# Kernel optimization log

Hardware: AMD Instinct MI355X
Metric: run time of the kernel (lower is better)

The kernel has to match this reference:

```python
import jax, jax.numpy as jnp
import numpy as np

H, DK = 16, 64
F = H * DK  # n_feat = 1024
B, T = 2, 2048


def setup_inputs() -> dict:
    key = jax.random.key(0)
    ks = jax.random.split(key, 11)
    mk = lambda k, sh: jax.random.normal(k, sh, dtype=jnp.float32)
    inp = {
        "query": mk(ks[0], (B, T, F)),
        "key": mk(ks[1], (B, T, F)),
        "value": mk(ks[2], (B, T, F)),
    }
    # Standard RoPE frequency table, shaped [T,1,1,DK] to broadcast over [t,b,h,d].
    pos = jnp.arange(T, dtype=jnp.float32)[:, None]
    inv_freq = 1.0 / (10000.0 ** (jnp.arange(0, DK, 2, dtype=jnp.float32) / DK))
    ang = pos * inv_freq                       # [T, DK/2]
    emb = jnp.concatenate([ang, ang], axis=-1)  # [T, DK]
    inp["cos"] = jnp.cos(emb)[:, None, None, :]
    inp["sin"] = jnp.sin(emb)[:, None, None, :]
    scale = 1.0 / np.sqrt(F).astype(np.float32)
    for i, n in enumerate(["wq", "wk", "wv", "wo"]):
        inp[n] = mk(ks[3 + i], (F, F)) * scale  # torch Linear weight layout [out,in]
    for i, n in enumerate(["bq", "bk", "bv", "bo"]):
        inp[n] = mk(ks[7 + i], (F,)) * 0.01
    return inp


def _rtt_half(x):
    d = x.shape[-1]
    return jnp.concatenate([-x[..., d // 2:], x[..., :d // 2]], axis=-1)


def reference(query, key, value, cos, sin, wq, bq, wk, bk, wv, bv, wo, bo):
    b, t, f = query.shape
    h, d = H, DK
    # [b,t,f] -> [t,b,h,d] as in the torch code (RoPE applied pre-projection)
    to_tbhd = lambda x: jnp.swapaxes(x, 0, 1).reshape(t, b, h, d)
    q = to_tbhd(query)
    k = to_tbhd(key)
    c, s = cos[:t], sin[:t]
    q = q * c + _rtt_half(q) * s
    k = k * c + _rtt_half(k) * s
    back = lambda x: jnp.swapaxes(x.reshape(t, b, f), 0, 1)  # -> [b,t,f]
    q, k = back(q), back(k)
    lin = lambda x, w, bias: x @ w.T + bias
    Q = lin(q, wq, bq).reshape(b, t, h, d)
    K = lin(k, wk, bk).reshape(b, t, h, d)
    V = lin(value, wv, bv).reshape(b, t, h, d)
    scores = jnp.einsum('bqhd,bkhd->bhqk', Q, K) / jnp.sqrt(jnp.float32(d))
    attn = jax.nn.softmax(scores, axis=-1)
    o = jnp.einsum('bhqk,bkhd->bqhd', attn, V).reshape(b, t, f)
    return o @ wo.T + bo
```

## Files before the change

### kernel.cpp

```cpp
#include <hip/hip_runtime.h>
#include <hip/hip_bf16.h>

#define DEVI __device__ __forceinline__

typedef unsigned short u16;
typedef unsigned int u32;
typedef __attribute__((ext_vector_type(8))) short bf16x8;
typedef __attribute__((ext_vector_type(4))) short bf16x4;
typedef __attribute__((ext_vector_type(4))) float f32x4;

#define Bn 2
#define Tn 2048
#define Hn 16
#define Dn 64
#define Fn 1024

DEVI u16 tobf(float f) {
    __hip_bfloat16 h = __float2bfloat16(f);
    return __builtin_bit_cast(u16, h);
}
DEVI float frombf(u16 u) {
    return __builtin_bit_cast(float, ((u32)u) << 16);
}

DEVI f32x4 mfma16(bf16x8 a, bf16x8 b, f32x4 c) {
    return __builtin_amdgcn_mfma_f32_16x16x32_bf16(a, b, c, 0, 0, 0);
}

DEVI void gload_lds16(const u16* g, u16* l) {
    __builtin_amdgcn_global_load_lds(
        (const __attribute__((address_space(1))) void*)g,
        (__attribute__((address_space(3))) void*)l, 16, 0, 0);
}

__global__ __launch_bounds__(256) void k_prep(const float* __restrict__ q,
                                              const float* __restrict__ k,
                                              const float* __restrict__ v,
                                              const float* __restrict__ cosb,
                                              const float* __restrict__ sinb,
                                              const float* __restrict__ wq,
                                              const float* __restrict__ wk,
                                              const float* __restrict__ wv,
                                              const float* __restrict__ wo,
                                              u16* __restrict__ Aq,
                                              u16* __restrict__ Ak,
                                              u16* __restrict__ Av) {
    if (blockIdx.x < 4096) {
        unsigned idx = blockIdx.x * 256 + threadIdx.x;
        unsigned which = idx >> 19;
        unsigned r = idx & 0x7FFFFu;
        unsigned d0 = (r & 7u) << 2;
        unsigned h = (r >> 3) & 15u;
        unsigned t = (r >> 7) & 2047u;
        unsigned b = (r >> 18) & 1u;
        const float* src = which ? k : q;
        u16* dst = which ? Ak : Aq;
        size_t base = ((size_t)(b * Tn + t)) * Fn + h * Dn;
        float4 lo = *(const float4*)(src + base + d0);
        float4 hi = *(const float4*)(src + base + d0 + 32);
        float4 cl = *(const float4*)(cosb + (size_t)t * Dn + d0);
        float4 ch = *(const float4*)(cosb + (size_t)t * Dn + d0 + 32);
        float4 sl = *(const float4*)(sinb + (size_t)t * Dn + d0);
        float4 sh = *(const float4*)(sinb + (size_t)t * Dn + d0 + 32);
        bf16x4 olo, ohi;
        olo[0] = (short)tobf(lo.x * cl.x - hi.x * sl.x);
        olo[1] = (short)tobf(lo.y * cl.y - hi.y * sl.y);
        olo[2] = (short)tobf(lo.z * cl.z - hi.z * sl.z);
        olo[3] = (short)tobf(lo.w * cl.w - hi.w * sl.w);
        ohi[0] = (short)tobf(hi.x * ch.x + lo.x * sh.x);
        ohi[1] = (short)tobf(hi.y * ch.y + lo.y * sh.y);
        ohi[2] = (short)tobf(hi.z * ch.z + lo.z * sh.z);
        ohi[3] = (short)tobf(hi.w * ch.w + lo.w * sh.w);
        *(bf16x4*)(dst + base + d0) = olo;
        *(bf16x4*)(dst + base + d0 + 32) = ohi;
    } else {
        size_t i8 = (((size_t)blockIdx.x - 4096) * 256 + threadIdx.x) * 8;
        const size_t M4 = (size_t)4 << 20, M1 = (size_t)1 << 20;
        const float* src;
        size_t off;
        if (i8 < M4)              { src = v;  off = i8; }
        else if (i8 < M4 + M1)    { src = wq; off = i8 - M4; }
        else if (i8 < M4 + 2*M1)  { src = wk; off = i8 - M4 - M1; }
        else if (i8 < M4 + 3*M1)  { src = wv; off = i8 - M4 - 2*M1; }
        else                      { src = wo; off = i8 - M4 - 3*M1; }
        float4 a = *(const float4*)(src + off);
        float4 c = *(const float4*)(src + off + 4);
        bf16x8 vv;
        vv[0] = (short)tobf(a.x); vv[1] = (short)tobf(a.y);
        vv[2] = (short)tobf(a.z); vv[3] = (short)tobf(a.w);
        vv[4] = (short)tobf(c.x); vv[5] = (short)tobf(c.y);
        vv[6] = (short)tobf(c.z); vv[7] = (short)tobf(c.w);
        *(bf16x8*)(Av + i8) = vv;
    }
}

DEVI void store_out(u16* p, float v) { *p = tobf(v); }
DEVI void store_out(float* p, float v) { *p = v; }

template <typename OUT>
DEVI void gemm_body(const u16* __restrict__ A, const u16* __restrict__ W,
                    const float* __restrict__ bias, OUT* __restrict__ C,
                    float scale, u16* As, u16* Bs, int mode) {
    const int tid = threadIdx.x;
    const int lane = tid & 63;
    const int wave = tid >> 6;
    const int l15 = lane & 15, l4 = lane >> 4;
    const int bm = blockIdx.y << 7, bn = blockIdx.x << 7;
    const int wr = (wave >> 1) << 6, wc = (wave & 1) << 6;

    const int c0 = tid, c1 = tid + 256;
    const u16* A0p = A + (size_t)(bm + (c0 >> 2)) * 1024 + ((c0 & 3) << 3);
    const u16* A1p = A + (size_t)(bm + (c1 >> 2)) * 1024 + ((c1 & 3) << 3);
    const u16* B0p = W + (size_t)(bn + (c0 >> 2)) * 1024 + ((c0 & 3) << 3);
    const u16* B1p = W + (size_t)(bn + (c1 >> 2)) * 1024 + ((c1 & 3) << 3);
    u16* Ad0 = As + (c0 << 3);
    u16* Ad1 = As + (c1 << 3);
    u16* Bd0 = Bs + (c0 << 3);
    u16* Bd1 = Bs + (c1 << 3);

    f32x4 acc[4][4] = {};

    for (int k0 = 0; k0 < 1024; k0 += 32) {
        gload_lds16(A0p + k0, Ad0);
        gload_lds16(A1p + k0, Ad1);
        gload_lds16(B0p + k0, Bd0);
        gload_lds16(B1p + k0, Bd1);
        __syncthreads();
        bf16x8 af[4], bfr[4];
        #pragma unroll
        for (int m = 0; m < 4; m++)
            af[m] = *(const bf16x8*)(As + (wr + m * 16 + l15) * 32 + (l4 << 3));
        #pragma unroll
        for (int n = 0; n < 4; n++)
            bfr[n] = *(const bf16x8*)(Bs + (wc + n * 16 + l15) * 32 + (l4 << 3));
        #pragma unroll
        for (int m = 0; m < 4; m++)
            #pragma unroll
            for (int n = 0; n < 4; n++)
                acc[m][n] = mfma16(af[m], bfr[n], acc[m][n]);
        __syncthreads();
    }

    #pragma unroll
    for (int m = 0; m < 4; m++)
        #pragma unroll
        for (int n = 0; n < 4; n++) {
            const int gcol = bn + wc + n * 16 + l15;
            const float bb = bias[gcol];
            #pragma unroll
            for (int j = 0; j < 4; j++) {
                const int grow = bm + wr + m * 16 + (l4 << 2) + j;
                const float val = (acc[m][n][j] + bb) * scale;
                if (mode == 0) {
                    store_out(C + (size_t)grow * 1024 + gcol, val);
                } else {
                    const int b = grow >> 11, t = grow & 2047;
                    const int h = gcol >> 6, d = gcol & 63;
                    const int bh = b * 16 + h, tt2 = t >> 6, r = t & 63;
                    const size_t tbase = ((size_t)(bh * 32 + tt2)) << 12;
                    size_t off;
                    if (mode == 1) {
                        const int nn = ((r >> 5) << 1) | ((r >> 2) & 1);
                        const int kk = d >> 5, ll4 = (d >> 3) & 3, e = d & 7;
                        const int ll15 = (((r >> 3) & 3) << 2) | (r & 3);
                        off = tbase + ((size_t)(nn * 2 + kk) << 9) +
                              ((ll4 * 16 + ll15) << 3) + e;
                    } else {
                        const int kk = r >> 5, ll4 = (r >> 3) & 3, e = r & 7;
                        const int nd = d >> 4, ll15 = d & 15;
                        off = tbase + ((size_t)(kk * 4 + nd) << 9) +
                              ((ll4 * 16 + ll15) << 3) + e;
                    }
                    ((u16*)C)[off] = tobf(val);
                }
            }
        }
}

__global__ __launch_bounds__(256) void k_gemm_qkv(
    const u16* A0, const u16* W0, const float* b0, u16* C0,
    const u16* A1, const u16* W1, const float* b1, u16* C1,
    const u16* A2, const u16* W2, const float* b2, u16* C2) {
    __shared__ __align__(16) u16 As[128 * 32];
    __shared__ __align__(16) u16 Bs[128 * 32];
    const int z = blockIdx.z;
    const u16* A = z == 0 ? A0 : (z == 1 ? A1 : A2);
    const u16* W = z == 0 ? W0 : (z == 1 ? W1 : W2);
    const float* bias = z == 0 ? b0 : (z == 1 ? b1 : b2);
    u16* C = z == 0 ? C0 : (z == 1 ? C1 : C2);
    const float scale = z == 0 ? 0.125f * 1.4426950408889634f : 1.0f;
    gemm_body<u16>(A, W, bias, C, scale, As, Bs, z);
}

__global__ __launch_bounds__(256) void k_gemm_f32(const u16* __restrict__ A,
                                                  const u16* __restrict__ W,
                                                  const float* __restrict__ bias,
                                                  float* __restrict__ C) {
    __shared__ __align__(16) u16 As[128 * 32];
    __shared__ __align__(16) u16 Bs[128 * 32];
    gemm_body<float>(A, W, bias, C, 1.0f, As, Bs, 0);
}

__global__ __launch_bounds__(256) void k_attn(const u16* __restrict__ Qp,
                                              const u16* __restrict__ Kr,
                                              const u16* __restrict__ Vr,
                                              u16* __restrict__ Op0,
                                              u16* __restrict__ Op1,
                                              float* __restrict__ Ls) {
    const int tid = threadIdx.x, wave = tid >> 6, lane = tid & 63;
    const int l15 = lane & 15, l4 = lane >> 4;
    const int bh = blockIdx.x, b = bh >> 4, h = bh & 15;
    const int sp = blockIdx.z;
    const int q0 = blockIdx.y * 128 + wave * 32;
    const int tbase = sp << 4;

    bf16x8 aq[2][2];
    #pragma unroll
    for (int mq = 0; mq < 2; mq++)
        #pragma unroll
        for (int kk = 0; kk < 2; kk++)
            aq[mq][kk] = *(const bf16x8*)(Qp +
                ((size_t)(b * Tn + q0 + mq * 16 + l15)) * Fn + h * Dn + kk * 32 + (l4 << 3));

    f32x4 o[2][4] = {};
    float lrun[2] = {0.f, 0.f};

    bf16x8 ones;
    #pragma unroll
    for (int j = 0; j < 8; j++) ones[j] = (short)0x3F80;

    const u16* Kbr = Kr + ((size_t)bh << 17);
    const u16* Vbr = Vr + ((size_t)bh << 17);
    const int lo8 = lane * 8;

    bf16x8 ka[4][2];
    #pragma unroll
    for (int n = 0; n < 4; n++)
        #pragma unroll
        for (int kk = 0; kk < 2; kk++)
            ka[n][kk] = *(const bf16x8*)(Kbr + ((tbase * 8 + n * 2 + kk) << 9) + lo8);

    #pragma unroll 1
    for (int tt = 0; tt < 16; tt++) {
        const int tg = tbase + tt;
        bf16x8 va[2][4];
        #pragma unroll
        for (int kk = 0; kk < 2; kk++)
            #pragma unroll
            for (int nd = 0; nd < 4; nd++)
                va[kk][nd] = *(const bf16x8*)(Vbr + ((tg * 8 + kk * 4 + nd) << 9) + lo8);
        const int tn = (tt < 15) ? tg + 1 : tbase;
        bf16x8 kn[4][2];
        #pragma unroll
        for (int n = 0; n < 4; n++)
            #pragma unroll
            for (int kk = 0; kk < 2; kk++)
                kn[n][kk] = *(const bf16x8*)(Kbr + ((tn * 8 + n * 2 + kk) << 9) + lo8);

        f32x4 s[2][4] = {};
        __builtin_amdgcn_s_setprio(1);
        #pragma unroll
        for (int n = 0; n < 4; n++)
            #pragma unroll
            for (int kk = 0; kk < 2; kk++) {
                s[0][n] = mfma16(ka[n][kk], aq[0][kk], s[0][n]);
                s[1][n] = mfma16(ka[n][kk], aq[1][kk], s[1][n]);
            }
        __builtin_amdgcn_s_setprio(0);

        bf16x8 pb[2][2];
        #pragma unroll
        for (int mq = 0; mq < 2; mq++)
            #pragma unroll
            for (int kk = 0; kk < 2; kk++) {
                float p0 = __builtin_amdgcn_exp2f(s[mq][2 * kk][0]);
                float p1 = __builtin_amdgcn_exp2f(s[mq][2 * kk][1]);
                float p2 = __builtin_amdgcn_exp2f(s[mq][2 * kk][2]);
                float p3 = __builtin_amdgcn_exp2f(s[mq][2 * kk][3]);
                float p4 = __builtin_amdgcn_exp2f(s[mq][2 * kk + 1][0]);
                float p5 = __builtin_amdgcn_exp2f(s[mq][2 * kk + 1][1]);
                float p6 = __builtin_amdgcn_exp2f(s[mq][2 * kk + 1][2]);
                float p7 = __builtin_amdgcn_exp2f(s[mq][2 * kk + 1][3]);
                bf16x8 pv;
                pv[0] = (short)tobf(p0); pv[1] = (short)tobf(p1);
                pv[2] = (short)tobf(p2); pv[3] = (short)tobf(p3);
                pv[4] = (short)tobf(p4); pv[5] = (short)tobf(p5);
                pv[6] = (short)tobf(p6); pv[7] = (short)tobf(p7);
                pb[mq][kk] = pv;
            }

        f32x4 osum0 = {}, osum1 = {};
        __builtin_amdgcn_s_setprio(1);
        #pragma unroll
        for (int kk = 0; kk < 2; kk++) {
            #pragma unroll
            for (int nd = 0; nd < 4; nd++) {
                o[0][nd] = mfma16(va[kk][nd], pb[0][kk], o[0][nd]);
                o[1][nd] = mfma16(va[kk][nd], pb[1][kk], o[1][nd]);
            }
            osum0 = mfma16(ones, pb[0][kk], osum0);
            osum1 = mfma16(ones, pb[1][kk], osum1);
        }
        __builtin_amdgcn_s_setprio(0);
        lrun[0] += osum0[0];
        lrun[1] += osum1[0];

        #pragma unroll
        for (int n = 0; n < 4; n++) {
            ka[n][0] = kn[n][0];
            ka[n][1] = kn[n][1];
        }
    }

    u16* OpS = sp ? Op1 : Op0;
    #pragma unroll
    for (int mq = 0; mq < 2; mq++) {
        const int q = q0 + mq * 16 + l15;
        float inv = 1.f / lrun[mq];
        #pragma unroll
        for (int nd = 0; nd < 4; nd++) {
            bf16x4 ov;
            ov[0] = (short)tobf(o[mq][nd][0] * inv);
            ov[1] = (short)tobf(o[mq][nd][1] * inv);
            ov[2] = (short)tobf(o[mq][nd][2] * inv);
            ov[3] = (short)tobf(o[mq][nd][3] * inv);
            *(bf16x4*)(OpS + ((size_t)(b * Tn + q)) * Fn +
                       h * Dn + nd * 16 + (l4 << 2)) = ov;
        }
        if (l4 == 0)
            Ls[(((size_t)(sp * 2 + b)) * Tn + q) * Hn + h] = lrun[mq];
    }
}

__global__ __launch_bounds__(256) void k_combine(const u16* __restrict__ Op0,
                                                 const u16* __restrict__ Op1,
                                                 const float* __restrict__ Ls,
                                                 u16* __restrict__ Oa) {
    size_t e0 = ((size_t)blockIdx.x * 256 + threadIdx.x) * 8;
    int row = (int)(e0 >> 10);
    int b = row >> 11, q = row & 2047;
    int h = (int)(e0 >> 6) & 15;
    float l0 = Ls[(((size_t)(0 + b)) * Tn + q) * Hn + h];
    float l1 = Ls[(((size_t)(2 + b)) * Tn + q) * Hn + h];
    float inv = 1.f / (l0 + l1);
    float w0 = l0 * inv, w1 = l1 * inv;
    bf16x8 x0 = *(const bf16x8*)(Op0 + e0);
    bf16x8 x1 = *(const bf16x8*)(Op1 + e0);
    bf16x8 out;
    #pragma unroll
    for (int j = 0; j < 8; j++)
        out[j] = (short)tobf(frombf((u16)x0[j]) * w0 + frombf((u16)x1[j]) * w1);
    *(bf16x8*)(Oa + e0) = out;
}

extern "C" void kernel_launch(void* const* d_in, const int* in_sizes, int n_in,
                              void* d_out, int out_size, void* d_ws, size_t ws_size,
                              hipStream_t stream) {
    const float* q    = (const float*)d_in[0];
    const float* k    = (const float*)d_in[1];
    const float* v    = (const float*)d_in[2];
    const float* cosb = (const float*)d_in[3];
    const float* sinb = (const float*)d_in[4];
    const float* wq   = (const float*)d_in[5];
    const float* wk   = (const float*)d_in[6];
    const float* wv   = (const float*)d_in[7];
    const float* wo   = (const float*)d_in[8];
    const float* bq   = (const float*)d_in[9];
    const float* bk   = (const float*)d_in[10];
    const float* bv   = (const float*)d_in[11];
    const float* bo   = (const float*)d_in[12];

    char* ws = (char*)d_ws;
    const size_t MB = (size_t)1 << 20;
    u16* Aq  = (u16*)(ws);
    u16* Ak  = (u16*)(ws + 8 * MB);
    u16* Av  = (u16*)(ws + 16 * MB);
    u16* Wq  = (u16*)(ws + 24 * MB);
    u16* Wk  = (u16*)(ws + 26 * MB);
    u16* Wv  = (u16*)(ws + 28 * MB);
    u16* Wo  = (u16*)(ws + 30 * MB);
    u16* Qp  = (u16*)(ws + 32 * MB);
    u16* Kr  = (u16*)(ws + 40 * MB);
    u16* Vr  = (u16*)(ws + 48 * MB);
    float* Ls = (float*)Wq;
    u16* Op0 = Ak;
    u16* Op1 = Av;
    u16* Oa  = Aq;

    k_prep<<<8192, 256, 0, stream>>>(q, k, v, cosb, sinb, wq, wk, wv, wo,
                                     Aq, Ak, Av);
    k_gemm_qkv<<<dim3(8, 32, 3), 256, 0, stream>>>(Aq, Wq, bq, Qp,
                                                   Ak, Wk, bk, Kr,
                                                   Av, Wv, bv, Vr);
    k_attn<<<dim3(32, 16, 2), 256, 0, stream>>>(Qp, Kr, Vr, Op0, Op1, Ls);
    k_combine<<<2048, 256, 0, stream>>>(Op0, Op1, Ls, Oa);
    k_gemm_f32<<<dim3(8, 32), 256, 0, stream>>>(Oa, Wo, bo, (float*)d_out);
}
```

Measured before the change: 142.1 us.

## Split attention key range four ways and prefetch K directly into registers

The attention kernel now splits the key sequence into four chunks instead of two, doubling the grid and halving each block's loop length. The combine kernel merges four partial outputs weighted by their row sums. Partial buffers are relocated into the output buffer and freed workspace. The next K tile is loaded straight into the operand registers after the QK MFMAs, which removes the separate prefetch copy. The trade-off is more occupancy and parallelism against more partial-output traffic and a heavier combine pass.

```diff
diff --git a/kernel.cpp b/kernel.cpp
--- a/kernel.cpp
+++ b/kernel.cpp
@@ -206,13 +206,15 @@
                                               const u16* __restrict__ Vr,
                                               u16* __restrict__ Op0,
                                               u16* __restrict__ Op1,
+                                              u16* __restrict__ Op2,
+                                              u16* __restrict__ Op3,
                                               float* __restrict__ Ls) {
     const int tid = threadIdx.x, wave = tid >> 6, lane = tid & 63;
     const int l15 = lane & 15, l4 = lane >> 4;
     const int bh = blockIdx.x, b = bh >> 4, h = bh & 15;
     const int sp = blockIdx.z;
     const int q0 = blockIdx.y * 128 + wave * 32;
-    const int tbase = sp << 4;
+    const int tbase = sp << 3;
 
     bf16x8 aq[2][2];
     #pragma unroll
@@ -224,6 +226,7 @@
 
     f32x4 o[2][4] = {};
     float lrun[2] = {0.f, 0.f};
+    const f32x4 zero4 = {0.f, 0.f, 0.f, 0.f};
 
     bf16x8 ones;
     #pragma unroll
@@ -241,32 +244,32 @@
             ka[n][kk] = *(const bf16x8*)(Kbr + ((tbase * 8 + n * 2 + kk) << 9) + lo8);
 
     #pragma unroll 1
-    for (int tt = 0; tt < 16; tt++) {
+    for (int tt = 0; tt < 8; tt++) {
         const int tg = tbase + tt;
+        const int tn = (tt < 7) ? tg + 1 : tbase;
         bf16x8 va[2][4];
         #pragma unroll
         for (int kk = 0; kk < 2; kk++)
             #pragma unroll
             for (int nd = 0; nd < 4; nd++)
                 va[kk][nd] = *(const bf16x8*)(Vbr + ((tg * 8 + kk * 4 + nd) << 9) + lo8);
-        const int tn = (tt < 15) ? tg + 1 : tbase;
-        bf16x8 kn[4][2];
+
+        f32x4 s[2][4];
+        __builtin_amdgcn_s_setprio(1);
+        #pragma unroll
+        for (int n = 0; n < 4; n++) {
+            s[0][n] = mfma16(ka[n][0], aq[0][0], zero4);
+            s[1][n] = mfma16(ka[n][0], aq[1][0], zero4);
+            s[0][n] = mfma16(ka[n][1], aq[0][1], s[0][n]);
+            s[1][n] = mfma16(ka[n][1], aq[1][1], s[1][n]);
+        }
+        __builtin_amdgcn_s_setprio(0);
+
         #pragma unroll
         for (int n = 0; n < 4; n++)
             #pragma unroll
             for (int kk = 0; kk < 2; kk++)
-                kn[n][kk] = *(const bf16x8*)(Kbr + ((tn * 8 + n * 2 + kk) << 9) + lo8);
-
-        f32x4 s[2][4] = {};
-        __builtin_amdgcn_s_setprio(1);
-        #pragma unroll
-        for (int n = 0; n < 4; n++)
-            #pragma unroll
-            for (int kk = 0; kk < 2; kk++) {
-                s[0][n] = mfma16(ka[n][kk], aq[0][kk], s[0][n]);
-                s[1][n] = mfma16(ka[n][kk], aq[1][kk], s[1][n]);
-            }
-        __builtin_amdgcn_s_setprio(0);
+                ka[n][kk] = *(const bf16x8*)(Kbr + ((tn * 8 + n * 2 + kk) << 9) + lo8);
 
         bf16x8 pb[2][2];
         #pragma unroll
@@ -289,30 +292,24 @@
                 pb[mq][kk] = pv;
             }
 
-        f32x4 osum0 = {}, osum1 = {};
         __builtin_amdgcn_s_setprio(1);
-        #pragma unroll
-        for (int kk = 0; kk < 2; kk++) {
+        f32x4 osum0 = mfma16(ones, pb[0][0], zero4);
+        f32x4 osum1 = mfma16(ones, pb[1][0], zero4);
+        osum0 = mfma16(ones, pb[0][1], osum0);
+        osum1 = mfma16(ones, pb[1][1], osum1);
+        #pragma unroll
+        for (int kk = 0; kk < 2; kk++)
             #pragma unroll
             for (int nd = 0; nd < 4; nd++) {
                 o[0][nd] = mfma16(va[kk][nd], pb[0][kk], o[0][nd]);
                 o[1][nd] = mfma16(va[kk][nd], pb[1][kk], o[1][nd]);
             }
-            osum0 = mfma16(ones, pb[0][kk], osum0);
-            osum1 = mfma16(ones, pb[1][kk], osum1);
-        }
         __builtin_amdgcn_s_setprio(0);
         lrun[0] += osum0[0];
         lrun[1] += osum1[0];
-
-        #pragma unroll
-        for (int n = 0; n < 4; n++) {
-            ka[n][0] = kn[n][0];
-            ka[n][1] = kn[n][1];
-        }
     }
 
-    u16* OpS = sp ? Op1 : Op0;
+    u16* OpS = sp == 0 ? Op0 : (sp == 1 ? Op1 : (sp == 2 ? Op2 : Op3));
     #pragma unroll
     for (int mq = 0; mq < 2; mq++) {
         const int q = q0 + mq * 16 + l15;
@@ -334,6 +331,8 @@
 
 __global__ __launch_bounds__(256) void k_combine(const u16* __restrict__ Op0,
                                                  const u16* __restrict__ Op1,
+                                                 const u16* __restrict__ Op2,
+                                                 const u16* __restrict__ Op3,
                                                  const float* __restrict__ Ls,
                                                  u16* __restrict__ Oa) {
     size_t e0 = ((size_t)blockIdx.x * 256 + threadIdx.x) * 8;
@@ -342,14 +341,19 @@
     int h = (int)(e0 >> 6) & 15;
     float l0 = Ls[(((size_t)(0 + b)) * Tn + q) * Hn + h];
     float l1 = Ls[(((size_t)(2 + b)) * Tn + q) * Hn + h];
-    float inv = 1.f / (l0 + l1);
-    float w0 = l0 * inv, w1 = l1 * inv;
+    float l2 = Ls[(((size_t)(4 + b)) * Tn + q) * Hn + h];
+    float l3 = Ls[(((size_t)(6 + b)) * Tn + q) * Hn + h];
+    float inv = 1.f / (l0 + l1 + l2 + l3);
+    float w0 = l0 * inv, w1 = l1 * inv, w2 = l2 * inv, w3 = l3 * inv;
     bf16x8 x0 = *(const bf16x8*)(Op0 + e0);
     bf16x8 x1 = *(const bf16x8*)(Op1 + e0);
+    bf16x8 x2 = *(const bf16x8*)(Op2 + e0);
+    bf16x8 x3 = *(const bf16x8*)(Op3 + e0);
     bf16x8 out;
     #pragma unroll
     for (int j = 0; j < 8; j++)
-        out[j] = (short)tobf(frombf((u16)x0[j]) * w0 + frombf((u16)x1[j]) * w1);
+        out[j] = (short)tobf(frombf((u16)x0[j]) * w0 + frombf((u16)x1[j]) * w1 +
+                             frombf((u16)x2[j]) * w2 + frombf((u16)x3[j]) * w3);
     *(bf16x8*)(Oa + e0) = out;
 }
 
@@ -371,6 +375,7 @@
     const float* bo   = (const float*)d_in[12];
 
     char* ws = (char*)d_ws;
+    char* dob = (char*)d_out;
     const size_t MB = (size_t)1 << 20;
     u16* Aq  = (u16*)(ws);
     u16* Ak  = (u16*)(ws + 8 * MB);
@@ -382,17 +387,19 @@
     u16* Qp  = (u16*)(ws + 32 * MB);
     u16* Kr  = (u16*)(ws + 40 * MB);
     u16* Vr  = (u16*)(ws + 48 * MB);
-    float* Ls = (float*)Wq;
-    u16* Op0 = Ak;
-    u16* Op1 = Av;
-    u16* Oa  = Aq;
+    u16* Op0 = (u16*)(dob);
+    u16* Op1 = (u16*)(dob + 8 * MB);
+    u16* Op2 = (u16*)(ws);
+    u16* Op3 = (u16*)(ws + 8 * MB);
+    float* Ls = (float*)(ws + 16 * MB);
+    u16* Oa  = (u16*)(ws);
 
     k_prep<<<8192, 256, 0, stream>>>(q, k, v, cosb, sinb, wq, wk, wv, wo,
                                      Aq, Ak, Av);
     k_gemm_qkv<<<dim3(8, 32, 3), 256, 0, stream>>>(Aq, Wq, bq, Qp,
                                                    Ak, Wk, bk, Kr,
                                                    Av, Wv, bv, Vr);
-    k_attn<<<dim3(32, 16, 2), 256, 0, stream>>>(Qp, Kr, Vr, Op0, Op1, Ls);
-    k_combine<<<2048, 256, 0, stream>>>(Op0, Op1, Ls, Oa);
+    k_attn<<<dim3(32, 16, 4), 256, 0, stream>>>(Qp, Kr, Vr, Op0, Op1, Op2, Op3, Ls);
+    k_combine<<<2048, 256, 0, stream>>>(Op0, Op1, Op2, Op3, Ls, Oa);
     k_gemm_f32<<<dim3(8, 32), 256, 0, stream>>>(Oa, Wo, bo, (float*)d_out);
 }
```

New measurement: 146.4 us. 3.0% more time.
